# Kernel tuning notes

Measured on AMD Instinct MI355X. Metric: run time of the kernel, lower is better.

## Reference

```python
import jax, jax.numpy as jnp
import numpy as np

B, L, H, W, C = 4, 5, 32, 32, 256
M, D = 8, 32            # heads, dim_head
T, R = 2, 4             # num_types, num_relations
INNER = M * D


def setup_inputs() -> dict:
    key = jax.random.key(0)
    ks = jax.random.split(key, 16)
    x = jax.random.normal(ks[0], (B, L, H, W, C), jnp.float32)
    mask = jnp.ones((B, H, W, L, L), jnp.float32)
    types = jax.random.randint(ks[1], (B, L), 0, T)
    vel = jax.random.uniform(ks[2], (B, L), jnp.float32)
    dts = jax.random.randint(ks[3], (B, L), 0, 10).astype(jnp.float32)
    pe = jnp.broadcast_to(
        jnp.stack([vel, dts, types.astype(jnp.float32)], axis=-1)[:, :, None, None, :],
        (B, L, H, W, 3),
    )
    s = 0.02
    q_w = jax.random.normal(ks[4], (T, INNER, C), jnp.float32) * s
    q_b = jax.random.normal(ks[5], (T, INNER), jnp.float32) * s
    k_w = jax.random.normal(ks[6], (T, INNER, C), jnp.float32) * s
    k_b = jax.random.normal(ks[7], (T, INNER), jnp.float32) * s
    v_w = jax.random.normal(ks[8], (T, INNER, C), jnp.float32) * s
    v_b = jax.random.normal(ks[9], (T, INNER), jnp.float32) * s
    a_w = jax.random.normal(ks[10], (T, C, INNER), jnp.float32) * s
    a_b = jax.random.normal(ks[11], (T, C), jnp.float32) * s
    lim = float(np.sqrt(6.0 / (D + D)))
    relation_att = jax.random.uniform(ks[12], (R, M, D, D), jnp.float32, -lim, lim)
    relation_msg = jax.random.uniform(ks[13], (R, M, D, D), jnp.float32, -lim, lim)
    return dict(x=x, mask=mask, prior_encoding=pe,
                q_w=q_w, q_b=q_b, k_w=k_w, k_b=k_b, v_w=v_w, v_b=v_b,
                a_w=a_w, a_b=a_b, relation_att=relation_att, relation_msg=relation_msg)


def _split_heads(t):
    b, h, w, l, _ = t.shape
    return jnp.transpose(t.reshape(b, h, w, l, M, D), (0, 4, 1, 2, 3, 5))  # b m h w l d


def reference(x, mask, prior_encoding, q_w, q_b, k_w, k_b, v_w, v_b,
              a_w, a_b, relation_att, relation_msg):
    scale = D ** -0.5
    xb = jnp.transpose(x, (0, 2, 3, 1, 4))                 # b h w l c
    types = prior_encoding[:, :, 0, 0, 2].astype(jnp.int32)  # (b, l)

    def proj(Ws, bs):
        # gather per-type weights (same math as the one-hot einsum expansion)
        Wt = Ws[types]                                     # (b, l, o, c)
        bt = bs[types]                                     # (b, l, o)
        return jnp.einsum('bhwlc,bloc->bhwlo', xb, Wt) + bt[:, None, None]

    q = _split_heads(proj(q_w, q_b))
    k = _split_heads(proj(k_w, k_b))
    v = _split_heads(proj(v_w, v_b))                       # b m h w l d

    rel = types[:, :, None] * T + types[:, None, :]        # (b, i, j)
    w_att = jnp.transpose(relation_att[rel], (0, 3, 1, 2, 4, 5))  # b m i j d e
    w_msg = jnp.transpose(relation_msg[rel], (0, 3, 1, 2, 4, 5))

    att = jnp.einsum('bmhwip,bmijpq,bmhwjq->bmhwij', q, w_att, k) * scale
    att = jnp.where(mask[:, None] == 0, -jnp.inf, att)
    att = jax.nn.softmax(att, axis=-1)

    out = jnp.einsum('bmhwij,bmijpc,bmhwjp->bmhwic', att, w_msg, v)  # b m h w l d
    b, m, h, w, l, d = out.shape
    out = jnp.transpose(out, (0, 2, 3, 4, 1, 5)).reshape(b, h, w, l, m * d)

    Wa = a_w[types]                                        # (b, l, c, inner)
    ba = a_b[types]                                        # (b, l, c)
    out = jnp.einsum('bhwlc,bloc->bhwlo', out, Wa) + ba[:, None, None]
    # dropout is identity at inference
    return jnp.transpose(out, (0, 3, 1, 2, 4))             # b l h w c
```

## Files before the change

kernel.cpp:

```cpp
#include <hip/hip_runtime.h>
#include <hip/hip_bf16.h>

typedef unsigned short u16;
typedef unsigned int u32;
typedef __attribute__((ext_vector_type(4))) float f32x4;
typedef __attribute__((ext_vector_type(8))) short bf16x8;
typedef __attribute__((ext_vector_type(4))) unsigned int u32x4;
typedef __attribute__((ext_vector_type(8))) unsigned short u16x8;

#define DEV static __device__ __forceinline__


DEV u16 f2b(float f) {
  unsigned u = __float_as_uint(f);
  u = (u + 0x7FFFu + ((u >> 16) & 1u)) >> 16;
  return (u16)u;
}

__global__ __launch_bounds__(256) void prep_all_kernel(
    const float* __restrict__ x, const float* __restrict__ mask,
    const float* __restrict__ q_w, const float* __restrict__ q_b,
    const float* __restrict__ k_w, const float* __restrict__ k_b,
    const float* __restrict__ v_w, const float* __restrict__ v_b,
    const float* __restrict__ a_w,
    const float* __restrict__ r_att, const float* __restrict__ r_msg,
    u16* __restrict__ xbC, u32* __restrict__ maskB,
    u16* __restrict__ WbigC, float* __restrict__ Bbig, u16* __restrict__ awbC) {
  __shared__ u16 s[64 * 256];
  const int bid = blockIdx.x, tid = threadIdx.x;
  if (bid < 320) {
    const int bl = bid >> 4, rg = bid & 15;
    const float* xp = x + ((size_t)bl * 1024 + rg * 64) * 256;
    #pragma unroll
    for (int it = 0; it < 8; it++) {
      const int idx = (it * 256 + tid) * 8;
      const int row = idx >> 8;
      const int ch0 = (idx >> 3) & 31;
      f32x4 v0 = *(const f32x4*)(xp + idx);
      f32x4 v1 = *(const f32x4*)(xp + idx + 4);
      u16x8 o;
      o[0] = f2b(v0[0]); o[1] = f2b(v0[1]); o[2] = f2b(v0[2]); o[3] = f2b(v0[3]);
      o[4] = f2b(v1[0]); o[5] = f2b(v1[1]); o[6] = f2b(v1[2]); o[7] = f2b(v1[3]);
      *(u16x8*)&s[row * 256 + ((ch0 ^ (row & 31)) * 8)] = o;
    }
    __syncthreads();
    const int r = tid & 63;
    #pragma unroll
    for (int cc = 0; cc < 8; cc++) {
      const int ch = cc * 4 + (tid >> 6);
      u16x8 v = *(const u16x8*)&s[r * 256 + ((ch ^ (r & 31)) * 8)];
      *(u16x8*)(xbC + (((size_t)bl * 32 + ch) * 1024 + rg * 64 + r) * 8) = v;
    }
  } else if (bid < 336) {
    const int i2 = (bid - 320) * 256 + tid;
    const int b = i2 >> 10, r = i2 & 1023;
    const float* mp = mask + ((size_t)b * 1024 + r) * 25;
    u32 bits = 0;
    #pragma unroll
    for (int k = 0; k < 25; k++) bits |= (mp[k] == 0.f ? 1u : 0u) << k;
    maskB[i2] = bits;
  } else {
    int idx = (bid - 336) * 256 + tid;
    const int NW = 2 * 1280 * 256;
    if (idx < NW) {
      int t = idx / (1280 * 256);
      int o = (idx / 256) % 1280;
      int c = idx & 255;
      float val;
      if (o < 256) {
        val = k_w[(size_t)(t * 256 + o) * 256 + c];
        if (c == 0) Bbig[t * 1280 + o] = k_b[t * 256 + o];
      } else if (o < 768) {
        int sec = o - 256, tj = sec >> 8, q_ = sec & 255;
        int mh = q_ >> 5, qq = q_ & 31;
        const float* W = r_att + (size_t)((t * 2 + tj) * 8 + mh) * 1024;
        const float* qwc = q_w + (size_t)(t * 256 + mh * 32) * 256 + c;
        float sacc = 0.f;
        for (int p = 0; p < 32; p++) sacc += qwc[p * 256] * W[p * 32 + qq];
        val = sacc;
        if (c == 0) {
          float sb = 0.f;
          const float* qb = q_b + t * 256 + mh * 32;
          for (int p = 0; p < 32; p++) sb += qb[p] * W[p * 32 + qq];
          Bbig[t * 1280 + o] = sb;
        }
      } else {
        int sec = o - 768, ti = sec >> 8, c_ = sec & 255;
        int mh = c_ >> 5, cc = c_ & 31;
        const float* W = r_msg + (size_t)((ti * 2 + t) * 8 + mh) * 1024;
        const float* vwc = v_w + (size_t)(t * 256 + mh * 32) * 256 + c;
        float sacc = 0.f;
        for (int p = 0; p < 32; p++) sacc += vwc[p * 256] * W[p * 32 + cc];
        val = sacc;
        if (c == 0) {
          float sb = 0.f;
          const float* vb = v_b + t * 256 + mh * 32;
          for (int p = 0; p < 32; p++) sb += vb[p] * W[p * 32 + cc];
          Bbig[t * 1280 + o] = sb;
        }
      }
      WbigC[(((size_t)t * 32 + (c >> 3)) * 1280 + o) * 8 + (c & 7)] = f2b(val);
    } else {
      int k = idx - NW;
      if (k < 2 * 256 * 256) {
        int t2 = k >> 16, o2 = (k >> 8) & 255, c2 = k & 255;
        awbC[(((size_t)t2 * 32 + (c2 >> 3)) * 256 + o2) * 8 + (c2 & 7)] = f2b(a_w[k]);
      }
    }
  }
}

template <int NTOT, bool OUT_BF16, bool OUT_CHUNKED>
__global__ __launch_bounds__(256) void gemm_kernel(
    const u16* __restrict__ A, const u16* __restrict__ Wb,
    const float* __restrict__ bias, const float* __restrict__ pe,
    void* __restrict__ Out) {
  __shared__ u16 smem[16384];
  u16* a_lds = smem;
  u16* b_lds = smem + 8192;
  constexpr int NCT = NTOT / 128;
  const int lin = blockIdx.x;
  const int xcd = lin & 7;
  const int jj = lin >> 3;
  const int ct = jj % NCT;
  const int pl = jj / NCT;
  const int pair = xcd * 20 + pl;
  const int bl = pair >> 3, rt = pair & 7;

  const int t = (int)pe[(size_t)bl * 3072 + 2];
  const int tid = threadIdx.x, w = tid >> 6, lane = tid & 63;
  const int wm = w >> 1, wn = w & 1;
  const u16* Ab = A + (size_t)bl * 32 * 1024 * 8;
  const u16* Bb = Wb + (size_t)t * 32 * NTOT * 8;
  f32x4 acc[4][4] = {};
  const int r16 = lane & 15, kg8 = lane >> 4;

  float bv4[4];
  #pragma unroll
  for (int ni = 0; ni < 4; ni++)
    bv4[ni] = bias[t * NTOT + ct * 128 + wn * 64 + ni * 16 + r16];

  u32x4 ra[2][2], rb[2][2];
  #pragma unroll
  for (int pp = 0; pp < 2; pp++) {
    const int c = pp * 4 + w;
    #pragma unroll
    for (int h = 0; h < 2; h++) {
      ra[pp][h] = *(const u32x4*)(Ab + ((size_t)c * 1024 + rt * 128 + h * 64 + lane) * 8);
      rb[pp][h] = *(const u32x4*)(Bb + ((size_t)c * NTOT + ct * 128 + h * 64 + lane) * 8);
    }
  }
  #pragma unroll
  for (int kk = 0; kk < 8; kk++) {
    const int cs = kk & 1;
    #pragma unroll
    for (int h = 0; h < 2; h++) {
      *(u32x4*)&a_lds[cs * 4096 + (w * 128 + h * 64 + lane) * 8] = ra[cs][h];
      *(u32x4*)&b_lds[cs * 4096 + (w * 128 + h * 64 + lane) * 8] = rb[cs][h];
    }
    if (kk < 6) {
      const int c = (kk + 2) * 4 + w;
      #pragma unroll
      for (int h = 0; h < 2; h++) {
        ra[cs][h] = *(const u32x4*)(Ab + ((size_t)c * 1024 + rt * 128 + h * 64 + lane) * 8);
        rb[cs][h] = *(const u32x4*)(Bb + ((size_t)c * NTOT + ct * 128 + h * 64 + lane) * 8);
      }
    }
    __syncthreads();
    bf16x8 af[4], bfr[4];
    #pragma unroll
    for (int mi = 0; mi < 4; mi++)
      af[mi] = *(const bf16x8*)&a_lds[cs * 4096 + (kg8 * 128 + wm * 64 + mi * 16 + r16) * 8];
    #pragma unroll
    for (int ni = 0; ni < 4; ni++)
      bfr[ni] = *(const bf16x8*)&b_lds[cs * 4096 + (kg8 * 128 + wn * 64 + ni * 16 + r16) * 8];
    #pragma unroll
    for (int mi = 0; mi < 4; mi++)
      #pragma unroll
      for (int ni = 0; ni < 4; ni++)
        acc[mi][ni] =
            __builtin_amdgcn_mfma_f32_16x16x32_bf16(af[mi], bfr[ni], acc[mi][ni], 0, 0, 0);
  }
  __syncthreads();

  if constexpr (OUT_BF16) {
    #pragma unroll
    for (int mi = 0; mi < 4; mi++)
      #pragma unroll
      for (int ni = 0; ni < 4; ni++) {
        const int col_t = wn * 64 + ni * 16 + r16;
        const int ch = col_t >> 3, e = col_t & 7;
        #pragma unroll
        for (int rg = 0; rg < 4; rg++) {
          const int row_t = wm * 64 + mi * 16 + kg8 * 4 + rg;
          smem[row_t * 128 + ((ch ^ (row_t & 7)) << 3) + e] = f2b(acc[mi][ni][rg] + bv4[ni]);
        }
      }
    __syncthreads();
    u16* OutP = (u16*)Out;
    #pragma unroll
    for (int it = 0; it < 8; it++) {
      const int unit = it * 256 + tid;
      const int row = unit & 127, ch = unit >> 7;
      u16x8 v = *(const u16x8*)&smem[row * 128 + ((ch ^ (row & 7)) << 3)];
      *(u16x8*)(OutP + (((size_t)bl * (NTOT / 8) + ct * 16 + ch) * 1024 + rt * 128 + row) * 8) = v;
    }
  } else {
    float* OutF = (float*)Out;
    float* epf = (float*)(smem) + w * 2048;
    #pragma unroll
    for (int ph = 0; ph < 2; ph++) {
      if (ph) asm volatile("s_waitcnt lgkmcnt(0)" ::: "memory");
      #pragma unroll
      for (int m2 = 0; m2 < 2; m2++) {
        const int mi = ph * 2 + m2;
        #pragma unroll
        for (int ni = 0; ni < 4; ni++) {
          const int lcol = ni * 16 + r16;
          #pragma unroll
          for (int rg = 0; rg < 4; rg++) {
            const int lrow = m2 * 16 + kg8 * 4 + rg;
            epf[lrow * 64 + (lcol ^ ((lrow & 7) << 2))] = acc[mi][ni][rg] + bv4[ni];
          }
        }
      }
      asm volatile("s_waitcnt lgkmcnt(0)" ::: "memory");
      #pragma unroll
      for (int u = 0; u < 8; u++) {
        const int row = u * 4 + kg8;
        const int c4 = r16 * 4;
        f32x4 v = *(const f32x4*)&epf[row * 64 + (c4 ^ ((row & 7) << 2))];
        *(f32x4*)(OutF + ((size_t)bl * 1024 + rt * 128 + wm * 64 + ph * 32 + row) * NTOT +
                  ct * 128 + wn * 64 + c4) = v;
      }
    }
  }
}

DEV u32x4 ld16(const u16* p) { return *(const u32x4*)p; }
DEV void cvt8(u32x4 v, float* f) {
  #pragma unroll
  for (int e = 0; e < 4; e++) {
    f[2 * e]     = __uint_as_float(v[e] << 16);
    f[2 * e + 1] = __uint_as_float(v[e] & 0xffff0000u);
  }
}

__global__ __launch_bounds__(256) void attn_kernel(
    const u16* __restrict__ P, const u32* __restrict__ maskB,
    const float* __restrict__ pe, u16* __restrict__ AO) {
  const int m = blockIdx.y, b = blockIdx.z;
  const int tid = threadIdx.x, w = tid >> 6, lane = tid & 63;
  const int rt = blockIdx.x * 4 + w;
  const int r = rt * 16 + (lane & 15);
  const int ch = lane >> 4;
  const int cbk = m * 4 + ch;
  int tl[5];
  #pragma unroll
  for (int l = 0; l < 5; l++) tl[l] = (int)pe[(size_t)(b * 5 + l) * 3072 + 2];
  const float scale = 0.17677669529663687f;

  const u32 mb = maskB[b * 1024 + r];
  u32x4 kv[5], qav[5], qbv[5];
  #pragma unroll
  for (int j = 0; j < 5; j++)
    kv[j] = ld16(P + (((size_t)(b * 5 + j) * 160 + cbk) * 1024 + r) * 8);
  #pragma unroll
  for (int i = 0; i < 5; i++) {
    qav[i] = ld16(P + (((size_t)(b * 5 + i) * 160 + 32 + cbk) * 1024 + r) * 8);
    qbv[i] = ld16(P + (((size_t)(b * 5 + i) * 160 + 64 + cbk) * 1024 + r) * 8);
  }

  float kf[5][8];
  #pragma unroll
  for (int j = 0; j < 5; j++) cvt8(kv[j], kf[j]);

  float att[5][5];
  #pragma unroll
  for (int i = 0; i < 5; i++) {
    float qa[8], qb[8];
    cvt8(qav[i], qa);
    cvt8(qbv[i], qb);
    #pragma unroll
    for (int j = 0; j < 5; j++) {
      float s = 0.f;
      if (tl[j]) {
        #pragma unroll
        for (int e = 0; e < 8; e++) s += qb[e] * kf[j][e];
      } else {
        #pragma unroll
        for (int e = 0; e < 8; e++) s += qa[e] * kf[j][e];
      }
      att[i][j] = s;
    }
  }

  u32x4 vav[5], vbv[5];
  #pragma unroll
  for (int j = 0; j < 5; j++) {
    vav[j] = ld16(P + (((size_t)(b * 5 + j) * 160 + 96 + cbk) * 1024 + r) * 8);
    vbv[j] = ld16(P + (((size_t)(b * 5 + j) * 160 + 128 + cbk) * 1024 + r) * 8);
  }

  #pragma unroll
  for (int i = 0; i < 5; i++)
    #pragma unroll
    for (int j = 0; j < 5; j++) {
      float v = att[i][j];
      v += __shfl_xor(v, 16, 64);
      v += __shfl_xor(v, 32, 64);
      att[i][j] = v;
    }

  float p[5][5];
  #pragma unroll
  for (int i = 0; i < 5; i++) {
    float mx = -1e30f, a_[5];
    #pragma unroll
    for (int j = 0; j < 5; j++) {
      float a = att[i][j] * scale;
      if ((mb >> (i * 5 + j)) & 1) a = -1e30f;
      a_[j] = a;
      mx = fmaxf(mx, a);
    }
    float s = 0.f;
    #pragma unroll
    for (int j = 0; j < 5; j++) {
      float e = __expf(a_[j] - mx);
      p[i][j] = e;
      s += e;
    }
    const float inv = 1.f / s;
    #pragma unroll
    for (int j = 0; j < 5; j++) p[i][j] *= inv;
  }

  float acc[5][8] = {};
  #pragma unroll
  for (int j = 0; j < 5; j++) {
    float va[8], vb[8];
    cvt8(vav[j], va);
    cvt8(vbv[j], vb);
    #pragma unroll
    for (int i = 0; i < 5; i++) {
      const float pij = p[i][j];
      if (tl[i]) {
        #pragma unroll
        for (int e = 0; e < 8; e++) acc[i][e] += pij * vb[e];
      } else {
        #pragma unroll
        for (int e = 0; e < 8; e++) acc[i][e] += pij * va[e];
      }
    }
  }
  #pragma unroll
  for (int i = 0; i < 5; i++) {
    u16x8 o;
    #pragma unroll
    for (int e = 0; e < 8; e++) o[e] = f2b(acc[i][e]);
    *(u16x8*)(AO + (((size_t)(b * 5 + i) * 32 + cbk) * 1024 + r) * 8) = o;
  }
}

extern "C" void kernel_launch(void* const* d_in, const int* in_sizes, int n_in,
                              void* d_out, int out_size, void* d_ws, size_t ws_size,
                              hipStream_t stream) {
  const float* x     = (const float*)d_in[0];
  const float* mask  = (const float*)d_in[1];
  const float* pe    = (const float*)d_in[2];
  const float* q_w   = (const float*)d_in[3];
  const float* q_b   = (const float*)d_in[4];
  const float* k_w   = (const float*)d_in[5];
  const float* k_b   = (const float*)d_in[6];
  const float* v_w   = (const float*)d_in[7];
  const float* v_b   = (const float*)d_in[8];
  const float* a_w   = (const float*)d_in[9];
  const float* a_b   = (const float*)d_in[10];
  const float* r_att = (const float*)d_in[11];
  const float* r_msg = (const float*)d_in[12];

  char* ws = (char*)d_ws;
  u16*   xbC   = (u16*)(ws + 0);
  u16*   P     = (u16*)(ws + 10485760);
  u16*   AO    = (u16*)(ws + 62914560);
  u16*   WbigC = (u16*)(ws + 73400320);
  float* Bbig  = (float*)(ws + 74711040);
  u16*   awbC  = (u16*)(ws + 74721280);
  u32*   maskB = (u32*)(ws + 74983424);

  prep_all_kernel<<<dim3(3408), dim3(256), 0, stream>>>(
      x, mask, q_w, q_b, k_w, k_b, v_w, v_b, a_w, r_att, r_msg,
      xbC, maskB, WbigC, Bbig, awbC);
  gemm_kernel<1280, true, true><<<dim3(1600), dim3(256), 0, stream>>>(
      xbC, WbigC, Bbig, pe, (void*)P);
  attn_kernel<<<dim3(16, 8, 4), dim3(256), 0, stream>>>(P, maskB, pe, AO);
  gemm_kernel<256, false, false><<<dim3(320), dim3(256), 0, stream>>>(
      AO, awbC, a_b, pe, d_out);
}
```

Measured before the change: 66.02 us.

## Fuse fp32-to-bf16 conversion of x into the projection GEMM load path

Removes the prep stage that converted x to a chunked bf16 buffer. The first GEMM now reads fp32 x directly and converts it to bf16 in registers before storing to LDS. This saves a full extra read and write of the activation tensor and shrinks the prep launch. In exchange, the GEMM loads twice as many A bytes with strided per-row access and relies on L2 reuse across the column tiles.

```diff
diff --git a/kernel.cpp b/kernel.cpp
--- a/kernel.cpp
+++ b/kernel.cpp
@@ -18,41 +18,17 @@
 }
 
 __global__ __launch_bounds__(256) void prep_all_kernel(
-    const float* __restrict__ x, const float* __restrict__ mask,
+    const float* __restrict__ mask,
     const float* __restrict__ q_w, const float* __restrict__ q_b,
     const float* __restrict__ k_w, const float* __restrict__ k_b,
     const float* __restrict__ v_w, const float* __restrict__ v_b,
     const float* __restrict__ a_w,
     const float* __restrict__ r_att, const float* __restrict__ r_msg,
-    u16* __restrict__ xbC, u32* __restrict__ maskB,
+    u32* __restrict__ maskB,
     u16* __restrict__ WbigC, float* __restrict__ Bbig, u16* __restrict__ awbC) {
-  __shared__ u16 s[64 * 256];
   const int bid = blockIdx.x, tid = threadIdx.x;
-  if (bid < 320) {
-    const int bl = bid >> 4, rg = bid & 15;
-    const float* xp = x + ((size_t)bl * 1024 + rg * 64) * 256;
-    #pragma unroll
-    for (int it = 0; it < 8; it++) {
-      const int idx = (it * 256 + tid) * 8;
-      const int row = idx >> 8;
-      const int ch0 = (idx >> 3) & 31;
-      f32x4 v0 = *(const f32x4*)(xp + idx);
-      f32x4 v1 = *(const f32x4*)(xp + idx + 4);
-      u16x8 o;
-      o[0] = f2b(v0[0]); o[1] = f2b(v0[1]); o[2] = f2b(v0[2]); o[3] = f2b(v0[3]);
-      o[4] = f2b(v1[0]); o[5] = f2b(v1[1]); o[6] = f2b(v1[2]); o[7] = f2b(v1[3]);
-      *(u16x8*)&s[row * 256 + ((ch0 ^ (row & 31)) * 8)] = o;
-    }
-    __syncthreads();
-    const int r = tid & 63;
-    #pragma unroll
-    for (int cc = 0; cc < 8; cc++) {
-      const int ch = cc * 4 + (tid >> 6);
-      u16x8 v = *(const u16x8*)&s[r * 256 + ((ch ^ (r & 31)) * 8)];
-      *(u16x8*)(xbC + (((size_t)bl * 32 + ch) * 1024 + rg * 64 + r) * 8) = v;
-    }
-  } else if (bid < 336) {
-    const int i2 = (bid - 320) * 256 + tid;
+  if (bid < 16) {
+    const int i2 = bid * 256 + tid;
     const int b = i2 >> 10, r = i2 & 1023;
     const float* mp = mask + ((size_t)b * 1024 + r) * 25;
     u32 bits = 0;
@@ -60,7 +36,7 @@
     for (int k = 0; k < 25; k++) bits |= (mp[k] == 0.f ? 1u : 0u) << k;
     maskB[i2] = bits;
   } else {
-    int idx = (bid - 336) * 256 + tid;
+    int idx = (bid - 16) * 256 + tid;
     const int NW = 2 * 1280 * 256;
     if (idx < NW) {
       int t = idx / (1280 * 256);
@@ -110,9 +86,9 @@
   }
 }
 
-template <int NTOT, bool OUT_BF16, bool OUT_CHUNKED>
+template <int NTOT, bool OUT_BF16, bool A_FROM_X>
 __global__ __launch_bounds__(256) void gemm_kernel(
-    const u16* __restrict__ A, const u16* __restrict__ Wb,
+    const void* __restrict__ Asrc, const u16* __restrict__ Wb,
     const float* __restrict__ bias, const float* __restrict__ pe,
     void* __restrict__ Out) {
   __shared__ u16 smem[16384];
@@ -130,7 +106,8 @@
   const int t = (int)pe[(size_t)bl * 3072 + 2];
   const int tid = threadIdx.x, w = tid >> 6, lane = tid & 63;
   const int wm = w >> 1, wn = w & 1;
-  const u16* Ab = A + (size_t)bl * 32 * 1024 * 8;
+  const float* Xb = (const float*)Asrc + (size_t)bl * 1024 * 256;
+  const u16* Ab = (const u16*)Asrc + (size_t)bl * 32 * 1024 * 8;
   const u16* Bb = Wb + (size_t)t * 32 * NTOT * 8;
   f32x4 acc[4][4] = {};
   const int r16 = lane & 15, kg8 = lane >> 4;
@@ -140,13 +117,21 @@
   for (int ni = 0; ni < 4; ni++)
     bv4[ni] = bias[t * NTOT + ct * 128 + wn * 64 + ni * 16 + r16];
 
-  u32x4 ra[2][2], rb[2][2];
+  f32x4 raf[2][2][2];
+  u32x4 ra[2][2];
+  u32x4 rb[2][2];
   #pragma unroll
   for (int pp = 0; pp < 2; pp++) {
     const int c = pp * 4 + w;
     #pragma unroll
     for (int h = 0; h < 2; h++) {
-      ra[pp][h] = *(const u32x4*)(Ab + ((size_t)c * 1024 + rt * 128 + h * 64 + lane) * 8);
+      if constexpr (A_FROM_X) {
+        const float* xp = Xb + (size_t)(rt * 128 + h * 64 + lane) * 256 + c * 8;
+        raf[pp][h][0] = *(const f32x4*)xp;
+        raf[pp][h][1] = *(const f32x4*)(xp + 4);
+      } else {
+        ra[pp][h] = *(const u32x4*)(Ab + ((size_t)c * 1024 + rt * 128 + h * 64 + lane) * 8);
+      }
       rb[pp][h] = *(const u32x4*)(Bb + ((size_t)c * NTOT + ct * 128 + h * 64 + lane) * 8);
     }
   }
@@ -155,14 +140,30 @@
     const int cs = kk & 1;
     #pragma unroll
     for (int h = 0; h < 2; h++) {
-      *(u32x4*)&a_lds[cs * 4096 + (w * 128 + h * 64 + lane) * 8] = ra[cs][h];
+      if constexpr (A_FROM_X) {
+        u16x8 o;
+        #pragma unroll
+        for (int e = 0; e < 4; e++) {
+          o[e]     = f2b(raf[cs][h][0][e]);
+          o[e + 4] = f2b(raf[cs][h][1][e]);
+        }
+        *(u16x8*)&a_lds[cs * 4096 + (w * 128 + h * 64 + lane) * 8] = o;
+      } else {
+        *(u32x4*)&a_lds[cs * 4096 + (w * 128 + h * 64 + lane) * 8] = ra[cs][h];
+      }
       *(u32x4*)&b_lds[cs * 4096 + (w * 128 + h * 64 + lane) * 8] = rb[cs][h];
     }
     if (kk < 6) {
       const int c = (kk + 2) * 4 + w;
       #pragma unroll
       for (int h = 0; h < 2; h++) {
-        ra[cs][h] = *(const u32x4*)(Ab + ((size_t)c * 1024 + rt * 128 + h * 64 + lane) * 8);
+        if constexpr (A_FROM_X) {
+          const float* xp = Xb + (size_t)(rt * 128 + h * 64 + lane) * 256 + c * 8;
+          raf[cs][h][0] = *(const f32x4*)xp;
+          raf[cs][h][1] = *(const f32x4*)(xp + 4);
+        } else {
+          ra[cs][h] = *(const u32x4*)(Ab + ((size_t)c * 1024 + rt * 128 + h * 64 + lane) * 8);
+        }
         rb[cs][h] = *(const u32x4*)(Bb + ((size_t)c * NTOT + ct * 128 + h * 64 + lane) * 8);
       }
     }
@@ -380,7 +381,6 @@
   const float* r_msg = (const float*)d_in[12];
 
   char* ws = (char*)d_ws;
-  u16*   xbC   = (u16*)(ws + 0);
   u16*   P     = (u16*)(ws + 10485760);
   u16*   AO    = (u16*)(ws + 62914560);
   u16*   WbigC = (u16*)(ws + 73400320);
@@ -388,12 +388,12 @@
   u16*   awbC  = (u16*)(ws + 74721280);
   u32*   maskB = (u32*)(ws + 74983424);
 
-  prep_all_kernel<<<dim3(3408), dim3(256), 0, stream>>>(
-      x, mask, q_w, q_b, k_w, k_b, v_w, v_b, a_w, r_att, r_msg,
-      xbC, maskB, WbigC, Bbig, awbC);
+  prep_all_kernel<<<dim3(3088), dim3(256), 0, stream>>>(
+      mask, q_w, q_b, k_w, k_b, v_w, v_b, a_w, r_att, r_msg,
+      maskB, WbigC, Bbig, awbC);
   gemm_kernel<1280, true, true><<<dim3(1600), dim3(256), 0, stream>>>(
-      xbC, WbigC, Bbig, pe, (void*)P);
+      (const void*)x, WbigC, Bbig, pe, (void*)P);
   attn_kernel<<<dim3(16, 8, 4), dim3(256), 0, stream>>>(P, maskB, pe, AO);
   gemm_kernel<256, false, false><<<dim3(320), dim3(256), 0, stream>>>(
-      AO, awbC, a_b, pe, d_out);
-}
+      (const void*)AO, awbC, a_b, pe, d_out);
+}
```

After: 78.87 us. 19.5% more time.
